# Kernel tuning notes

Measured on AMD Instinct MI355X. Metric: run time of the kernel, lower is better.

Reference implementation:

```python
import jax, jax.numpy as jnp
import numpy as np

B_AUDIOS = 64      # num audios in batch
NODES    = 2048    # 5-frame chunks (nodes) per audio
IN, HID, OUT = 512, 256, 128
HEADS, NCLS  = 2, 7
NEG_SLOPE = 0.2    # PyG GATConv default


def setup_inputs() -> dict:
    key = jax.random.key(0)
    ks = jax.random.split(key, 12)
    N = B_AUDIOS * NODES
    # chain edges within each audio: i -> i+1 (local), offset per audio
    base = np.arange(NODES - 1)
    src = (base[None, :] + np.arange(B_AUDIOS)[:, None] * NODES).reshape(-1)
    edge_index = jnp.asarray(np.stack([src, src + 1]), dtype=jnp.int32)
    batch_indices = jnp.repeat(jnp.arange(B_AUDIOS, dtype=jnp.int32), NODES)
    s = 0.05
    return {
        "x": jax.random.normal(ks[0], (N, IN), jnp.float32),
        "edge_index": edge_index,
        "batch_indices": batch_indices,
        "num_audios": B_AUDIOS,
        "W1": jax.random.normal(ks[1], (HEADS * HID, IN)) * s,
        "as1": jax.random.normal(ks[2], (HEADS, HID)) * s,
        "ad1": jax.random.normal(ks[3], (HEADS, HID)) * s,
        "b1": jnp.zeros((HID,), jnp.float32),
        "W2": jax.random.normal(ks[4], (HEADS * OUT, HID)) * s,
        "as2": jax.random.normal(ks[5], (HEADS, OUT)) * s,
        "ad2": jax.random.normal(ks[6], (HEADS, OUT)) * s,
        "b2": jnp.zeros((OUT,), jnp.float32),
        "Wt": jax.random.normal(ks[7], (1, OUT)) * s,
        "bt": jnp.zeros((1,), jnp.float32),
        "Wa": jax.random.normal(ks[8], (2, OUT)) * s,
        "ba": jnp.zeros((2,), jnp.float32),
        "Wn": jax.random.normal(ks[9], (NCLS, OUT)) * s,
        "bn": jnp.zeros((NCLS,), jnp.float32),
    }


def _seg_softmax(e, seg, n):
    m = jax.ops.segment_max(e, seg, num_segments=n)
    ex = jnp.exp(e - m[seg])
    return ex / jax.ops.segment_sum(ex, seg, num_segments=n)[seg]


def _gat_conv(x, src, dst, W, a_src, a_dst, b):
    # PyG GATConv, heads=H, concat=False (head-mean), with self loops
    N = x.shape[0]
    H, C = a_src.shape
    loops = jnp.arange(N, dtype=src.dtype)
    s = jnp.concatenate([src, loops])
    d = jnp.concatenate([dst, loops])
    h = (x @ W.T).reshape(N, H, C)                      # [N,H,C]
    al_s = jnp.einsum('nhc,hc->nh', h, a_src)           # [N,H]
    al_d = jnp.einsum('nhc,hc->nh', h, a_dst)
    e = jax.nn.leaky_relu(al_s[s] + al_d[d], NEG_SLOPE)  # [E,H]
    alpha = _seg_softmax(e, d, N)                        # softmax over in-edges of dst
    out = jax.ops.segment_sum(alpha[:, :, None] * h[s], d, num_segments=N)
    return out.mean(axis=1) + b                          # concat=False -> head mean


def reference(x, edge_index, batch_indices, num_audios,
              W1, as1, ad1, b1, W2, as2, ad2, b2,
              Wt, bt, Wa, ba, Wn, bn):
    src, dst = edge_index[0], edge_index[1]
    # global GAT (gat1 -> relu -> gat2)
    h1 = jax.nn.relu(_gat_conv(x, src, dst, W1, as1, ad1, b1))
    emb = _gat_conv(h1, src, dst, W2, as2, ad2, b2)      # [N, OUT]
    node_pred = jax.nn.softmax(emb @ Wn.T + bn, axis=-1)
    # per-audio subgraph GAT: graphs are disjoint per-audio chains, so running the
    # same GATModel on each subgraph equals restricting the global embeddings.
    logit = (emb @ Wt.T + bt)[:, 0]                      # [N]
    w = _seg_softmax(logit, batch_indices, num_audios)   # per-audio temporal softmax
    attended = jax.ops.segment_sum(w[:, None] * emb, batch_indices,
                                   num_segments=num_audios)  # [B, OUT]
    audio_pred = attended @ Wa.T + ba                    # [B, 2]
    return node_pred, audio_pred
```

## Files before the change

### kernel.cpp

```cpp
#include <hip/hip_runtime.h>
#include <hip/hip_bf16.h>

typedef __bf16 bf16x8 __attribute__((ext_vector_type(8)));
typedef __bf16 bf16x4 __attribute__((ext_vector_type(4)));
typedef float f32x4 __attribute__((ext_vector_type(4)));

#define NTOT   131072
#define NODES_PER_AUDIO 2048
#define NAUDIO 64
#define POOL_CHUNKS 16
#define CHUNK_NODES (NODES_PER_AUDIO / POOL_CHUNKS)

__global__ __launch_bounds__(256)
void detect_dtype(const unsigned* __restrict__ x, int* __restrict__ flag)
{
    const int tid = threadIdx.x;
    int cnt = 0;
    for (int i = tid; i < 4096; i += 256) {
        unsigned e = (x[i] >> 7) & 0xFF;
        cnt += (e >= 100 && e <= 145) ? 1 : 0;
    }
    __shared__ int red[256];
    red[tid] = cnt; __syncthreads();
    for (int s = 128; s > 0; s >>= 1) {
        if (tid < s) red[tid] += red[tid + s];
        __syncthreads();
    }
    if (tid == 0) *flag = (red[0] > 3000) ? 1 : 0;
}

struct W14 { const void* s[14]; int n[14]; int off[14]; };

__global__ __launch_bounds__(256)
void convert_weights(W14 w, const int* __restrict__ flag, __bf16* __restrict__ wb)
{
    const int f = *flag;
    const int stride = gridDim.x * 256;
    for (int t = 0; t < 14; t++) {
        const void* src = w.s[t];
        __bf16* d = wb + w.off[t];
        for (int i = blockIdx.x * 256 + threadIdx.x; i < w.n[t]; i += stride)
            d[i] = f ? ((const __bf16*)src)[i] : (__bf16)((const float*)src)[i];
    }
}

__global__ __launch_bounds__(256)
void gemm_dyn(const void* __restrict__ Araw, const __bf16* __restrict__ W,
              __bf16* __restrict__ C, int M, int K, int Nc,
              const int* __restrict__ flagp)
{
    __shared__ __align__(16) __bf16 As[128 * 32];
    __shared__ __align__(16) __bf16 Bs[128 * 32];

    const int colBase = blockIdx.x * 128;
    const int rowBase = blockIdx.y * 128;
    const int tid  = threadIdx.x;
    const int wave = tid >> 6;
    const int lane = tid & 63;
    const int wrow = (wave >> 1) * 64;
    const int wcol = (wave & 1) * 64;
    const int lr = lane & 15;
    const int lq = lane >> 4;
    const int f = *flagp;

    f32x4 acc[4][4] = {};

    const int c0 = tid, c1 = tid + 256;
    const int r0 = c0 >> 2, q0 = c0 & 3;
    const int r1 = c1 >> 2, q1 = c1 & 3;
    const __bf16* A16 = (const __bf16*)Araw;
    const float*  A32 = (const float*)Araw;
    const __bf16* a0p = A16 + (size_t)(rowBase + r0) * K + q0 * 8;
    const __bf16* a1p = A16 + (size_t)(rowBase + r1) * K + q1 * 8;
    const float*  a0f = A32 + (size_t)(rowBase + r0) * K + q0 * 8;
    const float*  a1f = A32 + (size_t)(rowBase + r1) * K + q1 * 8;
    const __bf16* b0p = W + (size_t)(colBase + r0) * K + q0 * 8;
    const __bf16* b1p = W + (size_t)(colBase + r1) * K + q1 * 8;

    for (int k0 = 0; k0 < K; k0 += 32) {
        __syncthreads();
        __builtin_amdgcn_global_load_lds(
            (const __attribute__((address_space(1))) void*)(b0p + k0),
            (__attribute__((address_space(3))) void*)&Bs[c0 * 8], 16, 0, 0);
        __builtin_amdgcn_global_load_lds(
            (const __attribute__((address_space(1))) void*)(b1p + k0),
            (__attribute__((address_space(3))) void*)&Bs[c1 * 8], 16, 0, 0);
        if (f) {
            __builtin_amdgcn_global_load_lds(
                (const __attribute__((address_space(1))) void*)(a0p + k0),
                (__attribute__((address_space(3))) void*)&As[c0 * 8], 16, 0, 0);
            __builtin_amdgcn_global_load_lds(
                (const __attribute__((address_space(1))) void*)(a1p + k0),
                (__attribute__((address_space(3))) void*)&As[c1 * 8], 16, 0, 0);
        } else {
            float4 u0 = *(const float4*)(a0f + k0);
            float4 u1 = *(const float4*)(a0f + k0 + 4);
            float4 v0 = *(const float4*)(a1f + k0);
            float4 v1 = *(const float4*)(a1f + k0 + 4);
            __bf16 t0[8] = {(__bf16)u0.x, (__bf16)u0.y, (__bf16)u0.z, (__bf16)u0.w,
                            (__bf16)u1.x, (__bf16)u1.y, (__bf16)u1.z, (__bf16)u1.w};
            __bf16 t1[8] = {(__bf16)v0.x, (__bf16)v0.y, (__bf16)v0.z, (__bf16)v0.w,
                            (__bf16)v1.x, (__bf16)v1.y, (__bf16)v1.z, (__bf16)v1.w};
            *(int4*)&As[c0 * 8] = *(int4*)t0;
            *(int4*)&As[c1 * 8] = *(int4*)t1;
        }
        __syncthreads();

        bf16x8 af[4], bfr[4];
        #pragma unroll
        for (int i = 0; i < 4; i++)
            af[i] = *(const bf16x8*)&As[(wrow + i * 16 + lr) * 32 + lq * 8];
        #pragma unroll
        for (int j = 0; j < 4; j++)
            bfr[j] = *(const bf16x8*)&Bs[(wcol + j * 16 + lr) * 32 + lq * 8];
        #pragma unroll
        for (int i = 0; i < 4; i++)
            #pragma unroll
            for (int j = 0; j < 4; j++)
                acc[i][j] = __builtin_amdgcn_mfma_f32_16x16x32_bf16(
                    af[i], bfr[j], acc[i][j], 0, 0, 0);
    }

    #pragma unroll
    for (int i = 0; i < 4; i++) {
        #pragma unroll
        for (int j = 0; j < 4; j++) {
            int col = colBase + wcol + j * 16 + lr;
            #pragma unroll
            for (int r = 0; r < 4; r++) {
                int row = rowBase + wrow + i * 16 + lq * 4 + r;
                C[(size_t)row * Nc + col] = (__bf16)acc[i][j][r];
            }
        }
    }
}

__global__ __launch_bounds__(256)
void gemm_bt(const __bf16* __restrict__ A, const __bf16* __restrict__ W,
             __bf16* __restrict__ C, int M, int K, int Nc)
{
    __shared__ __align__(16) __bf16 As[128 * 32];
    __shared__ __align__(16) __bf16 Bs[128 * 32];

    const int colBase = blockIdx.x * 128;
    const int rowBase = blockIdx.y * 128;
    const int tid  = threadIdx.x;
    const int wave = tid >> 6;
    const int lane = tid & 63;
    const int wrow = (wave >> 1) * 64;
    const int wcol = (wave & 1) * 64;
    const int lr = lane & 15;
    const int lq = lane >> 4;

    f32x4 acc[4][4] = {};

    const int c0 = tid, c1 = tid + 256;
    const int r0 = c0 >> 2, q0 = c0 & 3;
    const int r1 = c1 >> 2, q1 = c1 & 3;
    const __bf16* a0p = A + (size_t)(rowBase + r0) * K + q0 * 8;
    const __bf16* a1p = A + (size_t)(rowBase + r1) * K + q1 * 8;
    const __bf16* b0p = W + (size_t)(colBase + r0) * K + q0 * 8;
    const __bf16* b1p = W + (size_t)(colBase + r1) * K + q1 * 8;

    for (int k0 = 0; k0 < K; k0 += 32) {
        __syncthreads();
        __builtin_amdgcn_global_load_lds(
            (const __attribute__((address_space(1))) void*)(a0p + k0),
            (__attribute__((address_space(3))) void*)&As[c0 * 8], 16, 0, 0);
        __builtin_amdgcn_global_load_lds(
            (const __attribute__((address_space(1))) void*)(a1p + k0),
            (__attribute__((address_space(3))) void*)&As[c1 * 8], 16, 0, 0);
        __builtin_amdgcn_global_load_lds(
            (const __attribute__((address_space(1))) void*)(b0p + k0),
            (__attribute__((address_space(3))) void*)&Bs[c0 * 8], 16, 0, 0);
        __builtin_amdgcn_global_load_lds(
            (const __attribute__((address_space(1))) void*)(b1p + k0),
            (__attribute__((address_space(3))) void*)&Bs[c1 * 8], 16, 0, 0);
        __syncthreads();

        bf16x8 af[4], bfr[4];
        #pragma unroll
        for (int i = 0; i < 4; i++)
            af[i] = *(const bf16x8*)&As[(wrow + i * 16 + lr) * 32 + lq * 8];
        #pragma unroll
        for (int j = 0; j < 4; j++)
            bfr[j] = *(const bf16x8*)&Bs[(wcol + j * 16 + lr) * 32 + lq * 8];
        #pragma unroll
        for (int i = 0; i < 4; i++)
            #pragma unroll
            for (int j = 0; j < 4; j++)
                acc[i][j] = __builtin_amdgcn_mfma_f32_16x16x32_bf16(
                    af[i], bfr[j], acc[i][j], 0, 0, 0);
    }

    #pragma unroll
    for (int i = 0; i < 4; i++) {
        #pragma unroll
        for (int j = 0; j < 4; j++) {
            int col = colBase + wcol + j * 16 + lr;
            #pragma unroll
            for (int r = 0; r < 4; r++) {
                int row = rowBase + wrow + i * 16 + lq * 4 + r;
                C[(size_t)row * Nc + col] = (__bf16)acc[i][j][r];
            }
        }
    }
}

template<int C, bool RELU, bool FUSE_HEAD>
__global__ __launch_bounds__(256)
void agg_fused(const __bf16* __restrict__ h, const __bf16* __restrict__ a_s,
               const __bf16* __restrict__ a_d, const __bf16* __restrict__ bias,
               void* __restrict__ outv,
               const __bf16* __restrict__ Wn, const __bf16* __restrict__ bn,
               const __bf16* __restrict__ Wt, const __bf16* __restrict__ bt,
               void* __restrict__ node_pred, float* __restrict__ logit,
               const int* __restrict__ flag)
{
    constexpr int D = 2 * C;
    constexpr int V = D / 64;
    const int n = blockIdx.x * 4 + (threadIdx.x >> 6);
    const int lane = threadIdx.x & 63;
    const bool have_prev = (n & (NODES_PER_AUDIO - 1)) != 0;
    const size_t np = have_prev ? (size_t)(n - 1) : (size_t)n;
    const int base = lane * V;

    __bf16 h0v[V], h1v[V];
    if constexpr (V == 8) {
        *(int4*)h0v = *(const int4*)(h + (size_t)n * D + base);
        *(int4*)h1v = *(const int4*)(h + np * D + base);
    } else {
        *(int2*)h0v = *(const int2*)(h + (size_t)n * D + base);
        *(int2*)h1v = *(const int2*)(h + np * D + base);
    }

    float ps = 0.f, pd = 0.f, pp = 0.f;
    #pragma unroll
    for (int j = 0; j < V; j++) {
        float av = (float)a_s[base + j], dv = (float)a_d[base + j];
        float x0 = (float)h0v[j], x1 = (float)h1v[j];
        ps += x0 * av; pd += x0 * dv; pp += x1 * av;
    }
    #pragma unroll
    for (int off = 1; off < 32; off <<= 1) {
        ps += __shfl_xor(ps, off, 64);
        pd += __shfl_xor(pd, off, 64);
        pp += __shfl_xor(pp, off, 64);
    }

    float es = ps + pd;  es = es > 0.f ? es : 0.2f * es;
    float a_self = 1.f, a_prev = 0.f;
    if (have_prev) {
        float ep = pp + pd;  ep = ep > 0.f ? ep : 0.2f * ep;
        float m = fmaxf(es, ep);
        float wsx = __expf(es - m), wpx = __expf(ep - m);
        float inv = 1.f / (wsx + wpx);
        a_self = wsx * inv; a_prev = wpx * inv;
    }

    const int cb = (lane & 31) * V;
    float outj[V];
    #pragma unroll
    for (int j = 0; j < V; j++) {
        float p = a_self * (float)h0v[j] + a_prev * (float)h1v[j];
        p = 0.5f * (p + __shfl_xor(p, 32, 64));
        p += (float)bias[cb + j];
        if (RELU) p = fmaxf(p, 0.f);
        outj[j] = p;
    }

    if constexpr (!FUSE_HEAD) {
        if (lane < 32) {
            __bf16 ov[V];
            #pragma unroll
            for (int j = 0; j < V; j++) ov[j] = (__bf16)outj[j];
            if constexpr (V == 8)
                *(int4*)((__bf16*)outv + (size_t)n * C + cb) = *(int4*)ov;
            else
                *(int2*)((__bf16*)outv + (size_t)n * C + cb) = *(int2*)ov;
        }
    } else {
        if (lane < 32)
            *(float4*)((float*)outv + (size_t)n * C + cb) = *(float4*)outj;

        float acc[8];
        #pragma unroll
        for (int k = 0; k < 7; k++) {
            float a = 0.f;
            #pragma unroll
            for (int j = 0; j < V; j++)
                a += outj[j] * (float)Wn[k * C + cb + j];
            acc[k] = a;
        }
        {
            float a = 0.f;
            #pragma unroll
            for (int j = 0; j < V; j++)
                a += outj[j] * (float)Wt[cb + j];
            acc[7] = a;
        }
        #pragma unroll
        for (int off = 1; off < 32; off <<= 1)
            #pragma unroll
            for (int k = 0; k < 8; k++)
                acc[k] += __shfl_xor(acc[k], off, 64);

        if (lane == 0) {
            float lg[7], m = -1e30f;
            #pragma unroll
            for (int k = 0; k < 7; k++) {
                lg[k] = acc[k] + (float)bn[k];
                m = fmaxf(m, lg[k]);
            }
            float s = 0.f;
            #pragma unroll
            for (int k = 0; k < 7; k++) { lg[k] = __expf(lg[k] - m); s += lg[k]; }
            float inv = 1.f / s;
            if (*flag) {
                #pragma unroll
                for (int k = 0; k < 7; k++)
                    ((__bf16*)node_pred)[(size_t)n * 7 + k] = (__bf16)(lg[k] * inv);
            } else {
                #pragma unroll
                for (int k = 0; k < 7; k++)
                    ((float*)node_pred)[(size_t)n * 7 + k] = lg[k] * inv;
            }
            logit[n] = acc[7] + (float)bt[0];
        }
    }
}

__global__ __launch_bounds__(256)
void audio_stats(const float* __restrict__ logit, float2* __restrict__ stats)
{
    const int b = blockIdx.x;
    const int tid = threadIdx.x;
    __shared__ float red[256];
    const float* lg = logit + b * NODES_PER_AUDIO;

    float m = -1e30f;
    for (int i = tid; i < NODES_PER_AUDIO; i += 256) m = fmaxf(m, lg[i]);
    red[tid] = m; __syncthreads();
    for (int s = 128; s > 0; s >>= 1) {
        if (tid < s) red[tid] = fmaxf(red[tid], red[tid + s]);
        __syncthreads();
    }
    m = red[0]; __syncthreads();

    float s = 0.f;
    for (int i = tid; i < NODES_PER_AUDIO; i += 256) s += __expf(lg[i] - m);
    red[tid] = s; __syncthreads();
    for (int st = 128; st > 0; st >>= 1) {
        if (tid < st) red[tid] += red[tid + st];
        __syncthreads();
    }
    if (tid == 0) stats[b] = make_float2(m, 1.f / red[0]);
}

__global__ __launch_bounds__(256)
void audio_partial(const float* __restrict__ emb, const float* __restrict__ logit,
                   const float2* __restrict__ stats, float* __restrict__ partial)
{
    const int b = blockIdx.x >> 4;
    const int chunk = blockIdx.x & 15;
    const int tid = threadIdx.x;
    const int c = tid & 127, half = tid >> 7;
    const float m = stats[b].x, inv = stats[b].y;
    const float* lg = logit + b * NODES_PER_AUDIO;
    const float* eb = emb + (size_t)b * NODES_PER_AUDIO * 128;

    __shared__ float attbuf[256];
    const int n0 = chunk * CHUNK_NODES + half * (CHUNK_NODES / 2);
    float att = 0.f;
    for (int i = n0; i < n0 + CHUNK_NODES / 2; i++) {
        float w = __expf(lg[i] - m) * inv;
        att += w * eb[(size_t)i * 128 + c];
    }
    attbuf[tid] = att; __syncthreads();
    if (tid < 128)
        partial[(size_t)(b * POOL_CHUNKS + chunk) * 128 + tid] =
            attbuf[tid] + attbuf[tid + 128];
}

__global__ __launch_bounds__(64)
void audio_final(const float* __restrict__ partial, const __bf16* __restrict__ Wa,
                 const __bf16* __restrict__ ba, void* __restrict__ outbase,
                 const int* __restrict__ flag)
{
    const int b = blockIdx.x;
    const int lane = threadIdx.x;
    const float* pb = partial + (size_t)b * POOL_CHUNKS * 128;

    float a0 = 0.f, a1 = 0.f;
    #pragma unroll
    for (int k = 0; k < POOL_CHUNKS; k++) {
        a0 += pb[k * 128 + lane * 2];
        a1 += pb[k * 128 + lane * 2 + 1];
    }
    float p0 = a0 * (float)Wa[lane * 2]       + a1 * (float)Wa[lane * 2 + 1];
    float p1 = a0 * (float)Wa[128 + lane * 2] + a1 * (float)Wa[128 + lane * 2 + 1];
    #pragma unroll
    for (int off = 1; off < 64; off <<= 1) {
        p0 += __shfl_xor(p0, off, 64);
        p1 += __shfl_xor(p1, off, 64);
    }
    if (lane == 0) {
        float r0 = p0 + (float)ba[0];
        float r1 = p1 + (float)ba[1];
        if (*flag) {
            ((__bf16*)outbase)[(size_t)NTOT * 7 + b * 2 + 0] = (__bf16)r0;
            ((__bf16*)outbase)[(size_t)NTOT * 7 + b * 2 + 1] = (__bf16)r1;
        } else {
            ((float*)outbase)[(size_t)NTOT * 7 + b * 2 + 0] = r0;
            ((float*)outbase)[(size_t)NTOT * 7 + b * 2 + 1] = r1;
        }
    }
}

extern "C" void kernel_launch(void* const* d_in, const int* in_sizes, int n_in,
                              void* d_out, int out_size, void* d_ws, size_t ws_size,
                              hipStream_t stream)
{
    const void* x = d_in[0];
    char* ws = (char*)d_ws;
    const size_t N = NTOT;

    __bf16* h  = (__bf16*)ws;
    size_t off = N * 1024;
    __bf16* h1 = (__bf16*)(ws + off); off += N * 512;
    float* logit = (float*)(ws + off); off += N * 4;
    __bf16* wb = (__bf16*)(ws + off); off += 331008 * 2;
    int* flag = (int*)(ws + off); off += 16;
    float2* stats = (float2*)(ws + off); off += NAUDIO * sizeof(float2);
    float* partial = (float*)(ws + off); off += (size_t)NAUDIO * POOL_CHUNKS * 128 * 4;
    __bf16* g2 = h;
    float* emb = (float*)(ws + N * 512);

    const int O_W1 = 0,      O_W2 = 262144, O_as1 = 327680, O_ad1 = 328192;
    const int O_b1 = 328704, O_as2 = 328960, O_ad2 = 329216, O_b2 = 329472;
    const int O_Wt = 329600, O_bt = 329728, O_Wa = 329736, O_ba = 329992;
    const int O_Wn = 330000, O_bn = 330896;

    W14 w;
    const void* srcs[14] = { d_in[4], d_in[8], d_in[5], d_in[6], d_in[7],
                             d_in[9], d_in[10], d_in[11], d_in[12], d_in[13],
                             d_in[14], d_in[15], d_in[16], d_in[17] };
    const int ns[14]   = { 262144, 65536, 512, 512, 256, 256, 256, 128,
                           128, 1, 256, 2, 896, 7 };
    const int offs[14] = { O_W1, O_W2, O_as1, O_ad1, O_b1, O_as2, O_ad2, O_b2,
                           O_Wt, O_bt, O_Wa, O_ba, O_Wn, O_bn };
    for (int i = 0; i < 14; i++) { w.s[i] = srcs[i]; w.n[i] = ns[i]; w.off[i] = offs[i]; }

    const int nwb = NTOT / 4;

    detect_dtype<<<1, 256, 0, stream>>>((const unsigned*)x, flag);
    convert_weights<<<512, 256, 0, stream>>>(w, flag, wb);

    gemm_dyn<<<dim3(4, NTOT / 128), 256, 0, stream>>>(x, wb + O_W1, h,
                                                      NTOT, 512, 512, flag);
    agg_fused<256, true, false><<<nwb, 256, 0, stream>>>(
        h, wb + O_as1, wb + O_ad1, wb + O_b1, h1,
        nullptr, nullptr, nullptr, nullptr, nullptr, nullptr, flag);
    gemm_bt<<<dim3(2, NTOT / 128), 256, 0, stream>>>(h1, wb + O_W2, g2,
                                                     NTOT, 256, 256);
    agg_fused<128, false, true><<<nwb, 256, 0, stream>>>(
        g2, wb + O_as2, wb + O_ad2, wb + O_b2, emb,
        wb + O_Wn, wb + O_bn, wb + O_Wt, wb + O_bt, d_out, logit, flag);
    audio_stats<<<NAUDIO, 256, 0, stream>>>(logit, stats);
    audio_partial<<<NAUDIO * POOL_CHUNKS, 256, 0, stream>>>(emb, logit, stats, partial);
    audio_final<<<NAUDIO, 64, 0, stream>>>(partial, wb + O_Wa, wb + O_ba, d_out, flag);
}
```

Baseline: 691.7 us.

## Unify GEMMs into templated kernel with K=64 tiles and XCD-aware block mapping

```diff
diff --git a/kernel.cpp b/kernel.cpp
--- a/kernel.cpp
+++ b/kernel.cpp
@@ -2,7 +2,6 @@
 #include <hip/hip_bf16.h>
 
 typedef __bf16 bf16x8 __attribute__((ext_vector_type(8)));
-typedef __bf16 bf16x4 __attribute__((ext_vector_type(4)));
 typedef float f32x4 __attribute__((ext_vector_type(4)));
 
 #define NTOT   131072
@@ -44,16 +43,26 @@
     }
 }
 
-__global__ __launch_bounds__(256)
-void gemm_dyn(const void* __restrict__ Araw, const __bf16* __restrict__ W,
-              __bf16* __restrict__ C, int M, int K, int Nc,
-              const int* __restrict__ flagp)
-{
-    __shared__ __align__(16) __bf16 As[128 * 32];
-    __shared__ __align__(16) __bf16 Bs[128 * 32];
-
-    const int colBase = blockIdx.x * 128;
-    const int rowBase = blockIdx.y * 128;
+template<int NX, bool DYN>
+__global__ __launch_bounds__(256)
+void gemm_tile(const void* __restrict__ Araw, const __bf16* __restrict__ W,
+               __bf16* __restrict__ C, int M, int K, int Nc,
+               const int* __restrict__ flagp)
+{
+    __shared__ __align__(16) __bf16 As[128 * 64];
+    __shared__ __align__(16) __bf16 Bs[128 * 64];
+
+    const int nb  = gridDim.x;
+    const int ny  = nb / NX;
+    const int ypx = ny >> 3;
+    const int bid = blockIdx.x;
+    const int xcd = bid & 7;
+    const int local = bid >> 3;
+    const int by = xcd * ypx + local / NX;
+    const int bx = local % NX;
+
+    const int colBase = bx * 128;
+    const int rowBase = by * 128;
     const int tid  = threadIdx.x;
     const int wave = tid >> 6;
     const int lane = tid & 63;
@@ -61,136 +70,69 @@
     const int wcol = (wave & 1) * 64;
     const int lr = lane & 15;
     const int lq = lane >> 4;
-    const int f = *flagp;
+    int f = 1;
+    if constexpr (DYN) f = *flagp;
 
     f32x4 acc[4][4] = {};
 
-    const int c0 = tid, c1 = tid + 256;
-    const int r0 = c0 >> 2, q0 = c0 & 3;
-    const int r1 = c1 >> 2, q1 = c1 & 3;
     const __bf16* A16 = (const __bf16*)Araw;
     const float*  A32 = (const float*)Araw;
-    const __bf16* a0p = A16 + (size_t)(rowBase + r0) * K + q0 * 8;
-    const __bf16* a1p = A16 + (size_t)(rowBase + r1) * K + q1 * 8;
-    const float*  a0f = A32 + (size_t)(rowBase + r0) * K + q0 * 8;
-    const float*  a1f = A32 + (size_t)(rowBase + r1) * K + q1 * 8;
-    const __bf16* b0p = W + (size_t)(colBase + r0) * K + q0 * 8;
-    const __bf16* b1p = W + (size_t)(colBase + r1) * K + q1 * 8;
-
-    for (int k0 = 0; k0 < K; k0 += 32) {
+    const __bf16* ap[4]; const float* af32[4]; const __bf16* bp[4];
+    #pragma unroll
+    for (int i = 0; i < 4; i++) {
+        const int c = tid + 256 * i;
+        const int r = c >> 3, q = c & 7;
+        ap[i]   = A16 + (size_t)(rowBase + r) * K + q * 8;
+        af32[i] = A32 + (size_t)(rowBase + r) * K + q * 8;
+        bp[i]   = W   + (size_t)(colBase + r) * K + q * 8;
+    }
+
+    for (int k0 = 0; k0 < K; k0 += 64) {
         __syncthreads();
-        __builtin_amdgcn_global_load_lds(
-            (const __attribute__((address_space(1))) void*)(b0p + k0),
-            (__attribute__((address_space(3))) void*)&Bs[c0 * 8], 16, 0, 0);
-        __builtin_amdgcn_global_load_lds(
-            (const __attribute__((address_space(1))) void*)(b1p + k0),
-            (__attribute__((address_space(3))) void*)&Bs[c1 * 8], 16, 0, 0);
-        if (f) {
+        #pragma unroll
+        for (int i = 0; i < 4; i++) {
+            const int c = tid + 256 * i;
             __builtin_amdgcn_global_load_lds(
-                (const __attribute__((address_space(1))) void*)(a0p + k0),
-                (__attribute__((address_space(3))) void*)&As[c0 * 8], 16, 0, 0);
-            __builtin_amdgcn_global_load_lds(
-                (const __attribute__((address_space(1))) void*)(a1p + k0),
-                (__attribute__((address_space(3))) void*)&As[c1 * 8], 16, 0, 0);
+                (const __attribute__((address_space(1))) void*)(bp[i] + k0),
+                (__attribute__((address_space(3))) void*)&Bs[c * 8], 16, 0, 0);
+        }
+        if (!DYN || f) {
+            #pragma unroll
+            for (int i = 0; i < 4; i++) {
+                const int c = tid + 256 * i;
+                __builtin_amdgcn_global_load_lds(
+                    (const __attribute__((address_space(1))) void*)(ap[i] + k0),
+                    (__attribute__((address_space(3))) void*)&As[c * 8], 16, 0, 0);
+            }
         } else {
-            float4 u0 = *(const float4*)(a0f + k0);
-            float4 u1 = *(const float4*)(a0f + k0 + 4);
-            float4 v0 = *(const float4*)(a1f + k0);
-            float4 v1 = *(const float4*)(a1f + k0 + 4);
-            __bf16 t0[8] = {(__bf16)u0.x, (__bf16)u0.y, (__bf16)u0.z, (__bf16)u0.w,
-                            (__bf16)u1.x, (__bf16)u1.y, (__bf16)u1.z, (__bf16)u1.w};
-            __bf16 t1[8] = {(__bf16)v0.x, (__bf16)v0.y, (__bf16)v0.z, (__bf16)v0.w,
-                            (__bf16)v1.x, (__bf16)v1.y, (__bf16)v1.z, (__bf16)v1.w};
-            *(int4*)&As[c0 * 8] = *(int4*)t0;
-            *(int4*)&As[c1 * 8] = *(int4*)t1;
+            #pragma unroll
+            for (int i = 0; i < 4; i++) {
+                const int c = tid + 256 * i;
+                float4 u0 = *(const float4*)(af32[i] + k0);
+                float4 u1 = *(const float4*)(af32[i] + k0 + 4);
+                __bf16 t[8] = {(__bf16)u0.x, (__bf16)u0.y, (__bf16)u0.z, (__bf16)u0.w,
+                               (__bf16)u1.x, (__bf16)u1.y, (__bf16)u1.z, (__bf16)u1.w};
+                *(int4*)&As[c * 8] = *(int4*)t;
+            }
         }
         __syncthreads();
 
-        bf16x8 af[4], bfr[4];
         #pragma unroll
-        for (int i = 0; i < 4; i++)
-            af[i] = *(const bf16x8*)&As[(wrow + i * 16 + lr) * 32 + lq * 8];
-        #pragma unroll
-        for (int j = 0; j < 4; j++)
-            bfr[j] = *(const bf16x8*)&Bs[(wcol + j * 16 + lr) * 32 + lq * 8];
-        #pragma unroll
-        for (int i = 0; i < 4; i++)
+        for (int kk = 0; kk < 2; kk++) {
+            bf16x8 avf[4], bvf[4];
+            #pragma unroll
+            for (int i = 0; i < 4; i++)
+                avf[i] = *(const bf16x8*)&As[(wrow + i * 16 + lr) * 64 + kk * 32 + lq * 8];
             #pragma unroll
             for (int j = 0; j < 4; j++)
-                acc[i][j] = __builtin_amdgcn_mfma_f32_16x16x32_bf16(
-                    af[i], bfr[j], acc[i][j], 0, 0, 0);
-    }
-
-    #pragma unroll
-    for (int i = 0; i < 4; i++) {
-        #pragma unroll
-        for (int j = 0; j < 4; j++) {
-            int col = colBase + wcol + j * 16 + lr;
-            #pragma unroll
-            for (int r = 0; r < 4; r++) {
-                int row = rowBase + wrow + i * 16 + lq * 4 + r;
-                C[(size_t)row * Nc + col] = (__bf16)acc[i][j][r];
-            }
-        }
-    }
-}
-
-__global__ __launch_bounds__(256)
-void gemm_bt(const __bf16* __restrict__ A, const __bf16* __restrict__ W,
-             __bf16* __restrict__ C, int M, int K, int Nc)
-{
-    __shared__ __align__(16) __bf16 As[128 * 32];
-    __shared__ __align__(16) __bf16 Bs[128 * 32];
-
-    const int colBase = blockIdx.x * 128;
-    const int rowBase = blockIdx.y * 128;
-    const int tid  = threadIdx.x;
-    const int wave = tid >> 6;
-    const int lane = tid & 63;
-    const int wrow = (wave >> 1) * 64;
-    const int wcol = (wave & 1) * 64;
-    const int lr = lane & 15;
-    const int lq = lane >> 4;
-
-    f32x4 acc[4][4] = {};
-
-    const int c0 = tid, c1 = tid + 256;
-    const int r0 = c0 >> 2, q0 = c0 & 3;
-    const int r1 = c1 >> 2, q1 = c1 & 3;
-    const __bf16* a0p = A + (size_t)(rowBase + r0) * K + q0 * 8;
-    const __bf16* a1p = A + (size_t)(rowBase + r1) * K + q1 * 8;
-    const __bf16* b0p = W + (size_t)(colBase + r0) * K + q0 * 8;
-    const __bf16* b1p = W + (size_t)(colBase + r1) * K + q1 * 8;
-
-    for (int k0 = 0; k0 < K; k0 += 32) {
-        __syncthreads();
-        __builtin_amdgcn_global_load_lds(
-            (const __attribute__((address_space(1))) void*)(a0p + k0),
-            (__attribute__((address_space(3))) void*)&As[c0 * 8], 16, 0, 0);
-        __builtin_amdgcn_global_load_lds(
-            (const __attribute__((address_space(1))) void*)(a1p + k0),
-            (__attribute__((address_space(3))) void*)&As[c1 * 8], 16, 0, 0);
-        __builtin_amdgcn_global_load_lds(
-            (const __attribute__((address_space(1))) void*)(b0p + k0),
-            (__attribute__((address_space(3))) void*)&Bs[c0 * 8], 16, 0, 0);
-        __builtin_amdgcn_global_load_lds(
-            (const __attribute__((address_space(1))) void*)(b1p + k0),
-            (__attribute__((address_space(3))) void*)&Bs[c1 * 8], 16, 0, 0);
-        __syncthreads();
-
-        bf16x8 af[4], bfr[4];
-        #pragma unroll
-        for (int i = 0; i < 4; i++)
-            af[i] = *(const bf16x8*)&As[(wrow + i * 16 + lr) * 32 + lq * 8];
-        #pragma unroll
-        for (int j = 0; j < 4; j++)
-            bfr[j] = *(const bf16x8*)&Bs[(wcol + j * 16 + lr) * 32 + lq * 8];
-        #pragma unroll
-        for (int i = 0; i < 4; i++)
-            #pragma unroll
-            for (int j = 0; j < 4; j++)
-                acc[i][j] = __builtin_amdgcn_mfma_f32_16x16x32_bf16(
-                    af[i], bfr[j], acc[i][j], 0, 0, 0);
+                bvf[j] = *(const bf16x8*)&Bs[(wcol + j * 16 + lr) * 64 + kk * 32 + lq * 8];
+            #pragma unroll
+            for (int i = 0; i < 4; i++)
+                #pragma unroll
+                for (int j = 0; j < 4; j++)
+                    acc[i][j] = __builtin_amdgcn_mfma_f32_16x16x32_bf16(
+                        avf[i], bvf[j], acc[i][j], 0, 0, 0);
+        }
     }
 
     #pragma unroll
@@ -456,13 +398,13 @@
     detect_dtype<<<1, 256, 0, stream>>>((const unsigned*)x, flag);
     convert_weights<<<512, 256, 0, stream>>>(w, flag, wb);
 
-    gemm_dyn<<<dim3(4, NTOT / 128), 256, 0, stream>>>(x, wb + O_W1, h,
-                                                      NTOT, 512, 512, flag);
+    gemm_tile<4, true><<<4 * (NTOT / 128), 256, 0, stream>>>(
+        x, wb + O_W1, h, NTOT, 512, 512, flag);
     agg_fused<256, true, false><<<nwb, 256, 0, stream>>>(
         h, wb + O_as1, wb + O_ad1, wb + O_b1, h1,
         nullptr, nullptr, nullptr, nullptr, nullptr, nullptr, flag);
-    gemm_bt<<<dim3(2, NTOT / 128), 256, 0, stream>>>(h1, wb + O_W2, g2,
-                                                     NTOT, 256, 256);
+    gemm_tile<2, false><<<2 * (NTOT / 128), 256, 0, stream>>>(
+        h1, wb + O_W2, g2, NTOT, 256, 256, flag);
     agg_fused<128, false, true><<<nwb, 256, 0, stream>>>(
         g2, wb + O_as2, wb + O_ad2, wb + O_b2, emb,
         wb + O_Wn, wb + O_bn, wb + O_Wt, wb + O_bt, d_out, logit, flag);
```

Result: faster. 650.0 us (-6.0%).
